# Kernel optimization log

Measured on AMD Instinct MI355X. Metric: run time of the kernel, lower is better.

Reference implementation:

```python
import jax, jax.numpy as jnp
import numpy as np

N = 131072      # total nodes across batched molecular graphs
E = 524288      # directed edges (avg degree ~4)
G = 4096        # number of graphs in the batch
C_IN = 78       # atom feature dim
C_OUT = 128


def _init_linear(key, fan_in, fan_out):
    kw, kb = jax.random.split(key)
    s = 1.0 / np.sqrt(fan_in)
    W = jax.random.uniform(kw, (fan_in, fan_out), jnp.float32, -s, s)
    b = jax.random.uniform(kb, (fan_out,), jnp.float32, -s, s)
    return W, b


def setup_inputs() -> dict:
    key = jax.random.key(0)
    ks = jax.random.split(key, 8)
    x = jax.random.normal(ks[0], (N, C_IN), jnp.float32)
    edge_index = jax.random.randint(ks[1], (2, E), 0, N, dtype=jnp.int32)
    # sorted graph assignment, every graph non-empty (32 nodes per graph)
    batch = ((jnp.arange(N, dtype=jnp.int32) * G) // N).astype(jnp.int32)
    W1, b1 = _init_linear(ks[2], C_IN, C_IN)
    W2, b2 = _init_linear(ks[3], C_IN, 2 * C_IN)
    W3, b3 = _init_linear(ks[4], 2 * C_IN, 4 * C_IN)
    fcW, fcb = _init_linear(ks[5], 4 * C_IN, C_OUT)
    return {"x": x, "edge_index": edge_index, "batch": batch,
            "W1": W1, "b1": b1, "W2": W2, "b2": b2,
            "W3": W3, "b3": b3, "fcW": fcW, "fcb": fcb}


def _gcn_norm(edge_index, n):
    # PyG gcn_norm: add self-loops (weight 1), symmetric D^-1/2 A D^-1/2
    loop = jnp.arange(n, dtype=edge_index.dtype)
    src = jnp.concatenate([edge_index[0], loop])
    dst = jnp.concatenate([edge_index[1], loop])
    deg = jax.ops.segment_sum(jnp.ones_like(dst, jnp.float32), dst, num_segments=n)
    dis = jnp.where(deg > 0, jax.lax.rsqrt(jnp.maximum(deg, 1.0)), 0.0)
    norm = dis[src] * dis[dst]  # [E + N]
    return src, dst, norm


def _gcn_conv(h, W, b, src, dst, norm, n):
    h = h @ W                       # linear transform first (PyG order)
    msg = h[src] * norm[:, None]    # gather + edge-normalize
    agg = jax.ops.segment_sum(msg, dst, num_segments=n)  # scatter-add
    return agg + b


def reference(x, edge_index, batch, W1, b1, W2, b2, W3, b3, fcW, fcb):
    n = x.shape[0]
    src, dst, norm = _gcn_norm(edge_index, n)
    h = jax.nn.relu(_gcn_conv(x, W1, b1, src, dst, norm, n))
    h = jax.nn.relu(_gcn_conv(h, W2, b2, src, dst, norm, n))
    h = jax.nn.relu(_gcn_conv(h, W3, b3, src, dst, norm, n))
    pooled = jax.ops.segment_max(h, batch, num_segments=G)  # global max pool
    out = pooled @ fcW + fcb
    # dropout is identity in eval mode
    return out
```

## Files before the change

### kernel.cpp

```cpp
#include <hip/hip_runtime.h>

#define NN 131072
#define NE 524288
#define NG 4096

typedef __attribute__((ext_vector_type(8))) short bfx8;
typedef __attribute__((ext_vector_type(4))) float f32x4;

static __device__ __forceinline__ ushort f2bf(float f) {
    union { float f; unsigned u; } v; v.f = f;
    unsigned r = (v.u + 0x7fff + ((v.u >> 16) & 1)) >> 16;
    return (ushort)r;
}
static __device__ __forceinline__ float bf2f(short s) {
    union { unsigned u; float f; } v;
    v.u = ((unsigned)(ushort)s) << 16;
    return v.f;
}


__global__ void k_count(const int* __restrict__ dst, int* __restrict__ counts) {
    int e = blockIdx.x * blockDim.x + threadIdx.x;
    if (e < NE) atomicAdd(&counts[dst[e]], 1);
}

__global__ void k_dis(const int* __restrict__ counts, float* __restrict__ dis) {
    int i = blockIdx.x * blockDim.x + threadIdx.x;
    if (i < NN) dis[i] = rsqrtf((float)(counts[i] + 1));
}

__global__ void k_scanA(const int* __restrict__ in, int* __restrict__ out, int* __restrict__ bsum) {
    __shared__ int s[256];
    int t = threadIdx.x;
    int i = blockIdx.x * 256 + t;
    int v = in[i];
    s[t] = v;
    __syncthreads();
    for (int off = 1; off < 256; off <<= 1) {
        int x = (t >= off) ? s[t - off] : 0;
        __syncthreads();
        s[t] += x;
        __syncthreads();
    }
    out[i] = s[t] - v;
    if (t == 255) bsum[blockIdx.x] = s[t];
}

__global__ void k_scanB(int* __restrict__ bsum) {
    __shared__ int s[512];
    int t = threadIdx.x;
    int v = bsum[t];
    s[t] = v;
    __syncthreads();
    for (int off = 1; off < 512; off <<= 1) {
        int x = (t >= off) ? s[t - off] : 0;
        __syncthreads();
        s[t] += x;
        __syncthreads();
    }
    bsum[t] = s[t] - v;
}

__global__ void k_scanC(int* __restrict__ rowstart, const int* __restrict__ bsum) {
    int t = threadIdx.x;
    int i = blockIdx.x * 256 + t;
    rowstart[i] += bsum[blockIdx.x];
    if (i == 0) rowstart[NN] = NE;
}

__global__ void k_fill(const int* __restrict__ src, const int* __restrict__ dst,
                       const int* __restrict__ rowstart, int* __restrict__ cursor,
                       const float* __restrict__ dis,
                       int* __restrict__ col, float* __restrict__ wgt) {
    int e = blockIdx.x * blockDim.x + threadIdx.x;
    if (e >= NE) return;
    int s = src[e], d = dst[e];
    int pos = rowstart[d] + atomicAdd(&cursor[d], 1);
    col[pos] = s;
    wgt[pos] = dis[s] * dis[d];
}

template<int CI, int CO, int KP>
__global__ void k_prepW(const float* __restrict__ W, ushort* __restrict__ WT) {
    int idx = blockIdx.x * 256 + threadIdx.x;
    if (idx >= CO * KP) return;
    int n = idx / KP, k = idx - n * KP;
    float v = (k < CI) ? W[k * CO + n] : 0.0f;
    WT[idx] = f2bf(v);
}

__global__ void k_prepX(const float* __restrict__ x, ushort* __restrict__ xb) {
    int idx = blockIdx.x * 256 + threadIdx.x;
    int i = idx / 96, c = idx - i * 96;
    xb[idx] = (c < 78) ? f2bf(x[i * 78 + c]) : (ushort)0;
}


template<int KP, int LCH, int CO, int CPO, bool POOL>
__global__ __launch_bounds__(256)
void k_fused(const ushort* __restrict__ hin, const int* __restrict__ rowstart,
             const int* __restrict__ col, const float* __restrict__ wgt,
             const float* __restrict__ dis,
             const ushort* __restrict__ BT, const float* __restrict__ bias,
             const int* __restrict__ batch,
             ushort* __restrict__ hout, float* __restrict__ pooled) {
    constexpr int NCH = KP / 8;
    constexpr int LP  = LCH * 8;
    constexpr int NP  = (CO + 63) / 64;
    __shared__ ushort sA[64 * LP];

    const int tid  = threadIdx.x;
    const int row0 = blockIdx.x * 64;

    for (int id = tid; id < 64 * NCH; id += 256) {
        int r  = id / NCH, kc = id - r * NCH;
        int i  = row0 + r;
        int ch = kc * 8;
        const ushort* gb = hin + ch;

        float d = dis[i];
        bfx8 self = *(const bfx8*)(hin + (size_t)i * KP + ch);
        float acc[8];
        #pragma unroll
        for (int k = 0; k < 8; ++k) acc[k] = d * d * bf2f(self[k]);

        int j = rowstart[i], j1 = rowstart[i + 1];
        for (; j + 4 <= j1; j += 4) {
            int c0 = col[j], c1 = col[j + 1], c2 = col[j + 2], c3 = col[j + 3];
            float w0 = wgt[j], w1 = wgt[j + 1], w2 = wgt[j + 2], w3 = wgt[j + 3];
            bfx8 g0 = *(const bfx8*)(gb + (size_t)c0 * KP);
            bfx8 g1 = *(const bfx8*)(gb + (size_t)c1 * KP);
            bfx8 g2 = *(const bfx8*)(gb + (size_t)c2 * KP);
            bfx8 g3 = *(const bfx8*)(gb + (size_t)c3 * KP);
            #pragma unroll
            for (int k = 0; k < 8; ++k) {
                acc[k] = fmaf(w0, bf2f(g0[k]), acc[k]);
                acc[k] = fmaf(w1, bf2f(g1[k]), acc[k]);
                acc[k] = fmaf(w2, bf2f(g2[k]), acc[k]);
                acc[k] = fmaf(w3, bf2f(g3[k]), acc[k]);
            }
        }
        for (; j < j1; ++j) {
            int c = col[j];
            float w = wgt[j];
            bfx8 g = *(const bfx8*)(gb + (size_t)c * KP);
            #pragma unroll
            for (int k = 0; k < 8; ++k) acc[k] = fmaf(w, bf2f(g[k]), acc[k]);
        }

        bfx8 ov;
        #pragma unroll
        for (int k = 0; k < 8; ++k) ov[k] = (short)f2bf(acc[k]);
        int swz = (kc & ~7) | ((kc & 7) ^ (r & 7));
        *(bfx8*)(sA + r * LP + swz * 8) = ov;
    }
    __syncthreads();

    const int lane = tid & 63;
    const int wave = tid >> 6;
    const int wr = wave >> 1, wc = wave & 1;
    const int l15 = lane & 15, l4 = lane >> 4;
    const int r7 = l15 & 7;
    const int rowA0 = wr * 32 + l15;
    const int gbase = row0 + wr * 32;
    const int koff = l4 * 8;

    #pragma unroll
    for (int p = 0; p < NP; ++p) {
        const int bc0 = p * 64 + wc * 32 + l15;
        f32x4 acc[2][2] = {};
        #pragma unroll
        for (int ks = 0; ks < KP / 32; ++ks) {
            int chunk = l4 + ks * 4;
            int swz = (chunk & ~7) | ((chunk & 7) ^ r7);
            int off = swz * 8;
            bfx8 a0 = *(const bfx8*)(sA + rowA0 * LP + off);
            bfx8 a1 = *(const bfx8*)(sA + (rowA0 + 16) * LP + off);
            bfx8 b0 = {0,0,0,0,0,0,0,0}, b1 = {0,0,0,0,0,0,0,0};
            if (bc0 < CO)      b0 = *(const bfx8*)(BT + (size_t)bc0 * KP + koff + ks * 32);
            if (bc0 + 16 < CO) b1 = *(const bfx8*)(BT + (size_t)(bc0 + 16) * KP + koff + ks * 32);
            acc[0][0] = __builtin_amdgcn_mfma_f32_16x16x32_bf16(a0, b0, acc[0][0], 0, 0, 0);
            acc[0][1] = __builtin_amdgcn_mfma_f32_16x16x32_bf16(a0, b1, acc[0][1], 0, 0, 0);
            acc[1][0] = __builtin_amdgcn_mfma_f32_16x16x32_bf16(a1, b0, acc[1][0], 0, 0, 0);
            acc[1][1] = __builtin_amdgcn_mfma_f32_16x16x32_bf16(a1, b1, acc[1][1], 0, 0, 0);
        }

        if constexpr (POOL) {
            const bool uni = (batch[gbase] == batch[gbase + 31]);
            #pragma unroll
            for (int fn = 0; fn < 2; ++fn) {
                int cg = p * 64 + wc * 32 + fn * 16 + l15;
                bool cok = cg < CO;
                float bs = cok ? bias[cg] : 0.0f;
                if (uni) {
                    float m = -1e30f;
                    #pragma unroll
                    for (int fm = 0; fm < 2; ++fm)
                        #pragma unroll
                        for (int j = 0; j < 4; ++j)
                            m = fmaxf(m, acc[fm][fn][j]);
                    m = fmaxf(m, __shfl_xor(m, 16));
                    m = fmaxf(m, __shfl_xor(m, 32));
                    if (l4 == 0 && cok) {
                        int g = batch[gbase];
                        float v = fmaxf(m + bs, 0.0f);
                        atomicMax((int*)&pooled[g * CO + cg], __float_as_int(v));
                    }
                } else {
                    #pragma unroll
                    for (int fm = 0; fm < 2; ++fm)
                        #pragma unroll
                        for (int j = 0; j < 4; ++j) {
                            if (cok) {
                                int rg = gbase + fm * 16 + l4 * 4 + j;
                                int g = batch[rg];
                                float v = fmaxf(acc[fm][fn][j] + bs, 0.0f);
                                atomicMax((int*)&pooled[g * CO + cg], __float_as_int(v));
                            }
                        }
                }
            }
        } else {
            #pragma unroll
            for (int fn = 0; fn < 2; ++fn) {
                int cg = p * 64 + wc * 32 + fn * 16 + l15;
                if (cg >= CPO) continue;
                float bs = (cg < CO) ? bias[cg] : 0.0f;
                #pragma unroll
                for (int fm = 0; fm < 2; ++fm)
                    #pragma unroll
                    for (int j = 0; j < 4; ++j) {
                        int row = gbase + fm * 16 + l4 * 4 + j;
                        float v = (cg < CO) ? fmaxf(acc[fm][fn][j] + bs, 0.0f) : 0.0f;
                        hout[(size_t)row * CPO + cg] = f2bf(v);
                    }
            }
        }
    }
}


__global__ __launch_bounds__(256)
void k_fc(const float* __restrict__ pooled, const float* __restrict__ fcW,
          const float* __restrict__ fcb, float* __restrict__ out) {
    __shared__ float sp[8][312];
    const int tid = threadIdx.x;
    const int g0 = blockIdx.x * 8;

    for (int k = tid; k < 8 * 312; k += 256)
        ((float*)sp)[k] = pooled[(size_t)g0 * 312 + k];
    __syncthreads();

    const int half = tid >> 7;
    const int c = tid & 127;
    float b = fcb[c];
    float acc0 = b, acc1 = b, acc2 = b, acc3 = b;
    const float* wp = fcW + c;
    const float* p0 = sp[half * 4 + 0];
    const float* p1 = sp[half * 4 + 1];
    const float* p2 = sp[half * 4 + 2];
    const float* p3 = sp[half * 4 + 3];
    #pragma unroll 4
    for (int k = 0; k < 312; ++k) {
        float w = wp[(size_t)k * 128];
        acc0 = fmaf(p0[k], w, acc0);
        acc1 = fmaf(p1[k], w, acc1);
        acc2 = fmaf(p2[k], w, acc2);
        acc3 = fmaf(p3[k], w, acc3);
    }
    float* o = out + (size_t)(g0 + half * 4) * 128 + c;
    o[0] = acc0; o[128] = acc1; o[256] = acc2; o[384] = acc3;
}


extern "C" void kernel_launch(void* const* d_in, const int* in_sizes, int n_in,
                              void* d_out, int out_size, void* d_ws, size_t ws_size,
                              hipStream_t stream) {
    const float* x    = (const float*)d_in[0];
    const int*   ei   = (const int*)d_in[1];
    const int*   srcv = ei;
    const int*   dstv = ei + NE;
    const int*   batch = (const int*)d_in[2];
    const float* W1 = (const float*)d_in[3];
    const float* b1 = (const float*)d_in[4];
    const float* W2 = (const float*)d_in[5];
    const float* b2 = (const float*)d_in[6];
    const float* W3 = (const float*)d_in[7];
    const float* b3 = (const float*)d_in[8];
    const float* fcW = (const float*)d_in[9];
    const float* fcb = (const float*)d_in[10];
    float* out = (float*)d_out;

    char* ws = (char*)d_ws;
    size_t off = 0;
    auto take = [&](size_t bytes) -> void* {
        void* p = ws + off;
        off += (bytes + 255) & ~(size_t)255;
        return p;
    };
    int*    counts   = (int*)take((size_t)NN * 4);
    int*    rowstart = (int*)take((size_t)(NN + 1) * 4);
    int*    cursor   = (int*)take((size_t)NN * 4);
    float*  dis      = (float*)take((size_t)NN * 4);
    int*    bsum     = (int*)take(512 * 4);
    int*    col      = (int*)take((size_t)NE * 4);
    float*  wgt      = (float*)take((size_t)NE * 4);
    ushort* xb       = (ushort*)take((size_t)NN * 96 * 2);
    ushort* h1       = (ushort*)take((size_t)NN * 96 * 2);
    ushort* h2       = (ushort*)take((size_t)NN * 160 * 2);
    float*  pooled   = (float*)take((size_t)NG * 312 * 4);
    ushort* W1T      = (ushort*)take((size_t)78 * 96 * 2);
    ushort* W2T      = (ushort*)take((size_t)156 * 96 * 2);
    ushort* W3T      = (ushort*)take((size_t)312 * 160 * 2);

    hipMemsetAsync(counts, 0, (size_t)NN * 4, stream);
    hipMemsetAsync(cursor, 0, (size_t)NN * 4, stream);
    hipMemsetAsync(pooled, 0, (size_t)NG * 312 * 4, stream);

    k_count<<<NE / 256, 256, 0, stream>>>(dstv, counts);
    k_dis<<<NN / 256, 256, 0, stream>>>(counts, dis);
    k_scanA<<<NN / 256, 256, 0, stream>>>(counts, rowstart, bsum);
    k_scanB<<<1, 512, 0, stream>>>(bsum);
    k_scanC<<<NN / 256, 256, 0, stream>>>(rowstart, bsum);
    k_fill<<<NE / 256, 256, 0, stream>>>(srcv, dstv, rowstart, cursor, dis, col, wgt);

    k_prepW<78, 78, 96><<<(78 * 96 + 255) / 256, 256, 0, stream>>>(W1, W1T);
    k_prepW<78, 156, 96><<<(156 * 96 + 255) / 256, 256, 0, stream>>>(W2, W2T);
    k_prepW<156, 312, 160><<<(312 * 160 + 255) / 256, 256, 0, stream>>>(W3, W3T);
    k_prepX<<<NN * 96 / 256, 256, 0, stream>>>(x, xb);

    k_fused<96, 16, 78, 96, false><<<NN / 64, 256, 0, stream>>>(
        xb, rowstart, col, wgt, dis, W1T, b1, nullptr, h1, nullptr);
    k_fused<96, 16, 156, 160, false><<<NN / 64, 256, 0, stream>>>(
        h1, rowstart, col, wgt, dis, W2T, b2, nullptr, h2, nullptr);
    k_fused<160, 24, 312, 312, true><<<NN / 64, 256, 0, stream>>>(
        h2, rowstart, col, wgt, dis, W3T, b3, batch, nullptr, pooled);

    k_fc<<<NG / 8, 256, 0, stream>>>(pooled, fcW, fcb, out);
}
```

Before: 356.9 us.

## Stage block CSR edges in LDS and widen per-thread gather to 32 channels

Each block now loads its 64 rows' rowstart, column indices and edge weights into shared memory once, instead of every channel-chunk thread re-reading them from global memory. Each thread then handles 32 channels (four 16-byte loads) per neighbor rather than 8, with edges unrolled by two. This is meant to cut redundant index and weight loads and issue wider gathers per edge. In exchange the kernel uses more LDS and registers (32 float accumulators) and has fewer threads doing the aggregation, which may reduce occupancy and parallelism. It also assumes KP is a multiple of 32.

```diff
diff --git a/kernel.cpp b/kernel.cpp
--- a/kernel.cpp
+++ b/kernel.cpp
@@ -3,6 +3,7 @@
 #define NN 131072
 #define NE 524288
 #define NG 4096
+#define ECAP 1024
 
 typedef __attribute__((ext_vector_type(8))) short bfx8;
 typedef __attribute__((ext_vector_type(4))) float f32x4;
@@ -105,54 +106,111 @@
              const int* __restrict__ batch,
              ushort* __restrict__ hout, float* __restrict__ pooled) {
     constexpr int NCH = KP / 8;
+    constexpr int NG4 = NCH / 4;
     constexpr int LP  = LCH * 8;
     constexpr int NP  = (CO + 63) / 64;
     __shared__ ushort sA[64 * LP];
+    __shared__ int   sRS[65];
+    __shared__ int   sCol[ECAP];
+    __shared__ float sWgt[ECAP];
 
     const int tid  = threadIdx.x;
     const int row0 = blockIdx.x * 64;
 
-    for (int id = tid; id < 64 * NCH; id += 256) {
-        int r  = id / NCH, kc = id - r * NCH;
-        int i  = row0 + r;
-        int ch = kc * 8;
-        const ushort* gb = hin + ch;
-
-        float d = dis[i];
-        bfx8 self = *(const bfx8*)(hin + (size_t)i * KP + ch);
-        float acc[8];
-        #pragma unroll
-        for (int k = 0; k < 8; ++k) acc[k] = d * d * bf2f(self[k]);
-
-        int j = rowstart[i], j1 = rowstart[i + 1];
-        for (; j + 4 <= j1; j += 4) {
-            int c0 = col[j], c1 = col[j + 1], c2 = col[j + 2], c3 = col[j + 3];
-            float w0 = wgt[j], w1 = wgt[j + 1], w2 = wgt[j + 2], w3 = wgt[j + 3];
-            bfx8 g0 = *(const bfx8*)(gb + (size_t)c0 * KP);
-            bfx8 g1 = *(const bfx8*)(gb + (size_t)c1 * KP);
-            bfx8 g2 = *(const bfx8*)(gb + (size_t)c2 * KP);
-            bfx8 g3 = *(const bfx8*)(gb + (size_t)c3 * KP);
+    if (tid < 65) sRS[tid] = rowstart[row0 + tid];
+    __syncthreads();
+    const int base  = sRS[0];
+    const int total = sRS[64] - base;
+    const bool inLDS = (total <= ECAP);
+    if (inLDS) {
+        for (int e = tid; e < total; e += 256) {
+            sCol[e] = col[base + e];
+            sWgt[e] = wgt[base + e];
+        }
+    }
+    __syncthreads();
+
+    for (int id = tid; id < 64 * NG4; id += 256) {
+        int r = id / NG4, g = id - r * NG4;
+        int i = row0 + r;
+        const ushort* hrow = hin + (size_t)i * KP + g * 32;
+
+        float acc[32];
+        {
+            float dd = dis[i]; dd *= dd;
+            bfx8 s0 = *(const bfx8*)(hrow);
+            bfx8 s1 = *(const bfx8*)(hrow + 8);
+            bfx8 s2 = *(const bfx8*)(hrow + 16);
+            bfx8 s3 = *(const bfx8*)(hrow + 24);
             #pragma unroll
             for (int k = 0; k < 8; ++k) {
-                acc[k] = fmaf(w0, bf2f(g0[k]), acc[k]);
-                acc[k] = fmaf(w1, bf2f(g1[k]), acc[k]);
-                acc[k] = fmaf(w2, bf2f(g2[k]), acc[k]);
-                acc[k] = fmaf(w3, bf2f(g3[k]), acc[k]);
-            }
-        }
-        for (; j < j1; ++j) {
-            int c = col[j];
-            float w = wgt[j];
-            bfx8 g = *(const bfx8*)(gb + (size_t)c * KP);
+                acc[k]      = dd * bf2f(s0[k]);
+                acc[8 + k]  = dd * bf2f(s1[k]);
+                acc[16 + k] = dd * bf2f(s2[k]);
+                acc[24 + k] = dd * bf2f(s3[k]);
+            }
+        }
+        const int j0 = sRS[r] - base, j1 = sRS[r + 1] - base;
+
+        auto edges = [&](const auto* cp, const auto* wp) {
+            int j = j0;
+            for (; j + 2 <= j1; j += 2) {
+                int c0 = cp[j], c1 = cp[j + 1];
+                float w0 = wp[j], w1 = wp[j + 1];
+                const ushort* g0p = hin + (size_t)c0 * KP + g * 32;
+                const ushort* g1p = hin + (size_t)c1 * KP + g * 32;
+                bfx8 a0 = *(const bfx8*)(g0p);
+                bfx8 a1 = *(const bfx8*)(g0p + 8);
+                bfx8 a2 = *(const bfx8*)(g0p + 16);
+                bfx8 a3 = *(const bfx8*)(g0p + 24);
+                bfx8 b0 = *(const bfx8*)(g1p);
+                bfx8 b1 = *(const bfx8*)(g1p + 8);
+                bfx8 b2 = *(const bfx8*)(g1p + 16);
+                bfx8 b3 = *(const bfx8*)(g1p + 24);
+                #pragma unroll
+                for (int k = 0; k < 8; ++k) {
+                    acc[k]      = fmaf(w0, bf2f(a0[k]), acc[k]);
+                    acc[8 + k]  = fmaf(w0, bf2f(a1[k]), acc[8 + k]);
+                    acc[16 + k] = fmaf(w0, bf2f(a2[k]), acc[16 + k]);
+                    acc[24 + k] = fmaf(w0, bf2f(a3[k]), acc[24 + k]);
+                }
+                #pragma unroll
+                for (int k = 0; k < 8; ++k) {
+                    acc[k]      = fmaf(w1, bf2f(b0[k]), acc[k]);
+                    acc[8 + k]  = fmaf(w1, bf2f(b1[k]), acc[8 + k]);
+                    acc[16 + k] = fmaf(w1, bf2f(b2[k]), acc[16 + k]);
+                    acc[24 + k] = fmaf(w1, bf2f(b3[k]), acc[24 + k]);
+                }
+            }
+            for (; j < j1; ++j) {
+                int c = cp[j];
+                float w = wp[j];
+                const ushort* gp = hin + (size_t)c * KP + g * 32;
+                bfx8 a0 = *(const bfx8*)(gp);
+                bfx8 a1 = *(const bfx8*)(gp + 8);
+                bfx8 a2 = *(const bfx8*)(gp + 16);
+                bfx8 a3 = *(const bfx8*)(gp + 24);
+                #pragma unroll
+                for (int k = 0; k < 8; ++k) {
+                    acc[k]      = fmaf(w, bf2f(a0[k]), acc[k]);
+                    acc[8 + k]  = fmaf(w, bf2f(a1[k]), acc[8 + k]);
+                    acc[16 + k] = fmaf(w, bf2f(a2[k]), acc[16 + k]);
+                    acc[24 + k] = fmaf(w, bf2f(a3[k]), acc[24 + k]);
+                }
+            }
+        };
+        if (inLDS) edges(sCol, sWgt);
+        else       edges(col + base, wgt + base);
+
+        #pragma unroll
+        for (int q = 0; q < 4; ++q) {
+            int kc = g * 4 + q;
+            int swz = (kc & ~7) | ((kc & 7) ^ (r & 7));
+            bfx8 ov;
             #pragma unroll
-            for (int k = 0; k < 8; ++k) acc[k] = fmaf(w, bf2f(g[k]), acc[k]);
-        }
-
-        bfx8 ov;
-        #pragma unroll
-        for (int k = 0; k < 8; ++k) ov[k] = (short)f2bf(acc[k]);
-        int swz = (kc & ~7) | ((kc & 7) ^ (r & 7));
-        *(bfx8*)(sA + r * LP + swz * 8) = ov;
+            for (int k = 0; k < 8; ++k) ov[k] = (short)f2bf(acc[q * 8 + k]);
+            *(bfx8*)(sA + r * LP + swz * 8) = ov;
+        }
     }
     __syncthreads();
 
```

After: 359.5 us. Within noise of the previous version (+0.7%).
